# Optimization experiments

Hardware: AMD Instinct MI355X
Metric: run time of the kernel (lower is better)

Reference implementation:

```python
import jax, jax.numpy as jnp
import numpy as np

MODEL_DIM = 2048
NUM_HEADS = 32
HEAD_DIM = MODEL_DIM // NUM_HEADS
WINDOW = 512
THETA = 10000.0


def _rope_cos_sin(pos_offset, T, dim):
    # freqs_cis for positions [pos_offset, pos_offset+T); total_len <= MAX_SEQ_LEN so no rescale
    inv_freq = 1.0 / (THETA ** (jnp.arange(0, dim, 2, dtype=jnp.float32) / dim))  # [dim/2]
    t = jnp.arange(pos_offset, pos_offset + T, dtype=jnp.float32)                 # [T]
    ang = t[:, None] * inv_freq[None, :]                                          # [T, dim/2]
    return jnp.cos(ang), jnp.sin(ang)


def _apply_rope(x, cos, sin):
    # x: [B, H, T, Hd]; complex multiply on (even, odd) pairs, done in fp32 like torch code
    dt = x.dtype
    xr = x.astype(jnp.float32).reshape(*x.shape[:-1], -1, 2)
    a, b = xr[..., 0], xr[..., 1]
    c = cos[None, None, :, :]
    s = sin[None, None, :, :]
    out = jnp.stack([a * c - b * s, a * s + b * c], axis=-1).reshape(x.shape)
    return out.astype(dt)


def setup_inputs() -> dict:
    key = jax.random.key(0)
    ks = jax.random.split(key, 7)
    B, T, D = 16, 256, MODEL_DIM
    cache_len = 512
    wscale = 1.0 / np.sqrt(MODEL_DIM)
    return {
        "x": jax.random.normal(ks[0], (B, T, D), jnp.float32),
        "past_k": jax.random.normal(ks[1], (B, NUM_HEADS, cache_len, HEAD_DIM), jnp.float32),
        "past_v": jax.random.normal(ks[2], (B, NUM_HEADS, cache_len, HEAD_DIM), jnp.float32),
        "Wq": jax.random.normal(ks[3], (D, D), jnp.float32) * wscale,
        "Wk": jax.random.normal(ks[4], (D, D), jnp.float32) * wscale,
        "Wv": jax.random.normal(ks[5], (D, D), jnp.float32) * wscale,
        "Wo": jax.random.normal(ks[6], (D, D), jnp.float32) * wscale,
        "pos_offset": 512,
    }


def reference(x, past_k, past_v, Wq, Wk, Wv, Wo, pos_offset):
    B, T, D = x.shape
    H, Hd = NUM_HEADS, HEAD_DIM

    q = (x @ Wq.T).reshape(B, T, H, Hd).transpose(0, 2, 1, 3)   # [B,H,T,Hd]
    cur_k = (x @ Wk.T).reshape(B, T, H, Hd).transpose(0, 2, 1, 3)
    cur_v = (x @ Wv.T).reshape(B, T, H, Hd).transpose(0, 2, 1, 3)

    cos, sin = _rope_cos_sin(pos_offset, T, Hd)
    q = _apply_rope(q, cos, sin)
    k_rot = _apply_rope(cur_k, cos, sin)

    # KV-cache window trim (static shapes)
    cache_len = past_k.shape[2]
    sapa = max(0, cache_len - (WINDOW - T))
    k = jnp.concatenate([past_k[:, :, sapa:], k_rot], axis=2)   # [B,H,Sk,Hd]
    v = jnp.concatenate([past_v[:, :, sapa:], cur_v], axis=2)
    Sk = k.shape[2]
    past_len_visible = Sk - T

    # fp32 attention with windowed-causal mask, matching torch eager math
    scores = jnp.einsum('bhqd,bhkd->bhqk', q.astype(jnp.float32), k.astype(jnp.float32))
    scores = scores * (Hd ** -0.5)
    masked = jnp.arange(Sk)[None, :] > (jnp.arange(T)[:, None] + past_len_visible)  # [T,Sk]
    scores = jnp.where(masked[None, None], -jnp.inf, scores)
    attn = jax.nn.softmax(scores, axis=-1)
    out = jnp.einsum('bhqk,bhkd->bhqd', attn, v.astype(jnp.float32))
    out = out.transpose(0, 2, 1, 3).reshape(B, T, D) @ Wo.T
    out = out.astype(x.dtype)

    # new KV cache: full cache + UNrotated current k (faithful to source), trimmed to window
    new_k = jnp.concatenate([past_k, cur_k], axis=2)[:, :, -WINDOW:]
    new_v = jnp.concatenate([past_v, cur_v], axis=2)[:, :, -WINDOW:]
    return out, new_k, new_v
```

## Files before the change

kernel.cpp:

```cpp
#include <hip/hip_runtime.h>
#include <cstdint>
#include <cstddef>

typedef __attribute__((ext_vector_type(8))) __bf16 bf16x8;
typedef __attribute__((ext_vector_type(4))) float f32x4;

typedef const __attribute__((address_space(1))) unsigned int* gas1_t;
typedef __attribute__((address_space(3))) unsigned int* las3_t;

__device__ __forceinline__ unsigned short f2bf(float f) {
  unsigned int u = __float_as_uint(f);
  u += 0x7FFFu + ((u >> 16) & 1u);
  return (unsigned short)(u >> 16);
}
__device__ __forceinline__ float bf2f(unsigned short h) {
  return __uint_as_float(((unsigned int)h) << 16);
}

__device__ __forceinline__ int detect_f32(const unsigned short* det) {
  int cnt = 0;
#pragma unroll
  for (int i = 0; i < 32; ++i) {
    const unsigned int e = (det[2 * i] >> 7) & 0xFF;
    cnt += (e >= 115 && e <= 135) ? 1 : 0;
  }
  return cnt < 16;
}

__device__ __forceinline__ float loadf(const void* b, size_t i, int f32) {
  return f32 ? ((const float*)b)[i] : bf2f(((const unsigned short*)b)[i]);
}
__device__ __forceinline__ void storef(void* b, size_t i, float v, int f32) {
  if (f32) ((float*)b)[i] = v;
  else     ((unsigned short*)b)[i] = f2bf(v);
}
__device__ __forceinline__ bf16x8 load8(const void* base, size_t elem, int f32) {
  if (f32) {
    const float* p = (const float*)base + elem;
    const float4 a = *(const float4*)p;
    const float4 b = *(const float4*)(p + 4);
    bf16x8 r;
    unsigned short* q = (unsigned short*)&r;
    q[0] = f2bf(a.x); q[1] = f2bf(a.y); q[2] = f2bf(a.z); q[3] = f2bf(a.w);
    q[4] = f2bf(b.x); q[5] = f2bf(b.y); q[6] = f2bf(b.z); q[7] = f2bf(b.w);
    return r;
  }
  return *(const bf16x8*)((const unsigned short*)base + elem);
}

__global__ __launch_bounds__(256) void convert_kernel(
    const void* __restrict__ x,  const void* __restrict__ wq,
    const void* __restrict__ wk, const void* __restrict__ wv,
    const void* __restrict__ wo,
    unsigned short* __restrict__ xb, unsigned short* __restrict__ wqkv,
    unsigned short* __restrict__ wob, const unsigned short* __restrict__ det)
{
  const int f32 = detect_f32(det);
  int c = blockIdx.x * 256 + threadIdx.x;
#pragma unroll
  for (int it = 0; it < 3; ++it, c += 1048576) {
    bf16x8 v; unsigned short* dp;
    if (c < 1048576) {
      v = load8(x, (size_t)c << 3, f32);                     dp = xb   + ((size_t)c << 3);
    } else if (c < 1572864) {
      v = load8(wq, (size_t)(c - 1048576) << 3, f32);        dp = wqkv + ((size_t)(c - 1048576) << 3);
    } else if (c < 2097152) {
      v = load8(wk, (size_t)(c - 1572864) << 3, f32);        dp = wqkv + 4194304 + ((size_t)(c - 1572864) << 3);
    } else if (c < 2621440) {
      v = load8(wv, (size_t)(c - 2097152) << 3, f32);        dp = wqkv + 8388608 + ((size_t)(c - 2097152) << 3);
    } else {
      v = load8(wo, (size_t)(c - 2621440) << 3, f32);        dp = wob  + ((size_t)(c - 2621440) << 3);
    }
    *(bf16x8*)dp = v;
  }
}

__global__ __launch_bounds__(256) void gemm_bf16_kernel(
    const unsigned short* __restrict__ A,
    const unsigned short* __restrict__ W,
    void* __restrict__ c0,
    void* __restrict__ dko,
    const unsigned short* __restrict__ det,
    int route)
{
  __shared__ __align__(16) unsigned short As[128 * 64];
  __shared__ __align__(16) unsigned short Bs[128 * 64];
  const int f32 = detect_f32(det);

  const int tid  = threadIdx.x;
  const int lane = tid & 63;
  const int wave = tid >> 6;
  const int quad = lane >> 4;
  const int l16  = lane & 15;

  const int qq  = gridDim.x >> 3;
  const int swz = (blockIdx.x & 7) * qq + (blockIdx.x >> 3);
  const int mBase = (swz & 31) * 128;
  const int nBase = (swz >> 5) * 128;

  const int wm = (wave >> 1) * 64;
  const int wn = (wave & 1) * 64;
  const int r0w  = wave * 32;
  const int lrow = lane >> 3;
  const int lch  = (lane & 7) ^ lrow;

  f32x4 acc[4][4];
#pragma unroll
  for (int i = 0; i < 4; ++i)
#pragma unroll
    for (int j = 0; j < 4; ++j) acc[i][j] = f32x4{0.f, 0.f, 0.f, 0.f};

  const unsigned short* Abase = A + (size_t)mBase * 2048;
  const unsigned short* Wbase = W + (size_t)nBase * 2048;
  const int sa = l16 & 7;

  for (int kb = 0; kb < 2048; kb += 64) {
    __syncthreads();
#pragma unroll
    for (int ii = 0; ii < 4; ++ii) {
      const int r0 = r0w + ii * 8;
      const size_t goff = (size_t)(r0 + lrow) * 2048 + kb + lch * 8;
      __builtin_amdgcn_global_load_lds((gas1_t)(Abase + goff),
                                       (las3_t)(As + r0 * 64), 16, 0, 0);
      __builtin_amdgcn_global_load_lds((gas1_t)(Wbase + goff),
                                       (las3_t)(Bs + r0 * 64), 16, 0, 0);
    }
    __syncthreads();

    bf16x8 af[2][4], bfr[2][4];
#pragma unroll
    for (int i = 0; i < 4; ++i) {
      const char* pa = (const char*)As + (wm + i * 16 + l16) * 128;
      const char* pb = (const char*)Bs + (wn + i * 16 + l16) * 128;
      af[0][i]  = *(const bf16x8*)(pa + ((quad ^ sa) << 4));
      af[1][i]  = *(const bf16x8*)(pa + (((quad + 4) ^ sa) << 4));
      bfr[0][i] = *(const bf16x8*)(pb + ((quad ^ sa) << 4));
      bfr[1][i] = *(const bf16x8*)(pb + (((quad + 4) ^ sa) << 4));
    }
#pragma unroll
    for (int kk = 0; kk < 2; ++kk)
#pragma unroll
      for (int i = 0; i < 4; ++i)
#pragma unroll
        for (int j = 0; j < 4; ++j)
          acc[i][j] = __builtin_amdgcn_mfma_f32_16x16x32_bf16(af[kk][i], bfr[kk][j], acc[i][j], 0, 0, 0);
  }

#pragma unroll
  for (int i = 0; i < 4; ++i) {
#pragma unroll
    for (int j = 0; j < 4; ++j) {
#pragma unroll
      for (int r = 0; r < 4; ++r) {
        const int m = mBase + wm + i * 16 + quad * 4 + r;
        const int n = nBase + wn + j * 16 + l16;
        if (route == 0) {
          storef(c0, (size_t)m * 2048 + n, acc[i][j][r], f32);
        } else {
          const int b = m >> 8, t = m & 255;
          const int seg = n >> 11;
          const int nn = n & 2047;
          const int hh = nn >> 6, d = nn & 63;
          if (seg == 0) {
            ((unsigned short*)c0)[(((size_t)(b * 32 + hh)) * 256 + t) * 64 + d] =
                f2bf(acc[i][j][r]);
          } else {
            const size_t coff = (seg == 1) ? (size_t)8388608 : (size_t)25165824;
            storef(dko, coff + (((size_t)(b * 32 + hh)) * 512 + 256 + t) * 64 + d,
                   acc[i][j][r], f32);
          }
        }
      }
    }
  }
}

__global__ __launch_bounds__(256) void gemm_bt_kernel(
    const void* __restrict__ A, const void* __restrict__ W, void* __restrict__ C,
    const unsigned short* __restrict__ det,
    int amode, int wmode, int cmode, size_t coff,
    int N, int K, int mode, int S, int t0)
{
  __shared__ __align__(16) unsigned short As[128 * 32];
  __shared__ __align__(16) unsigned short Bs[128 * 32];
  const int f32  = detect_f32(det);
  const int af32 = amode & f32, wf32 = wmode & f32, cf32 = cmode & f32;

  const int tid  = threadIdx.x;
  const int lane = tid & 63;
  const int wave = tid >> 6;
  const int quad = lane >> 4;
  const int l16  = lane & 15;
  const int mBase = blockIdx.x * 128;
  const int nBase = blockIdx.y * 128;
  const int wm = (wave >> 1) * 64;
  const int wn = (wave & 1) * 64;

  const int row0 = tid >> 2,          kc0 = (tid & 3) << 3;
  const int row1 = (256 + tid) >> 2,  kc1 = ((256 + tid) & 3) << 3;

  f32x4 acc[4][4];
#pragma unroll
  for (int i = 0; i < 4; ++i)
#pragma unroll
    for (int j = 0; j < 4; ++j) acc[i][j] = f32x4{0.f, 0.f, 0.f, 0.f};

  for (int kb = 0; kb < K; kb += 32) {
    const bf16x8 a0 = load8(A, (size_t)(mBase + row0) * K + kb + kc0, af32);
    const bf16x8 a1 = load8(A, (size_t)(mBase + row1) * K + kb + kc1, af32);
    const bf16x8 b0 = load8(W, (size_t)(nBase + row0) * K + kb + kc0, wf32);
    const bf16x8 b1 = load8(W, (size_t)(nBase + row1) * K + kb + kc1, wf32);
    __syncthreads();
    *(bf16x8*)&As[(size_t)tid * 8]         = a0;
    *(bf16x8*)&As[(size_t)(256 + tid) * 8] = a1;
    *(bf16x8*)&Bs[(size_t)tid * 8]         = b0;
    *(bf16x8*)&Bs[(size_t)(256 + tid) * 8] = b1;
    __syncthreads();

    bf16x8 af[4], bfr[4];
#pragma unroll
    for (int i = 0; i < 4; ++i)
      af[i]  = *(const bf16x8*)&As[(wm + i * 16 + l16) * 32 + quad * 8];
#pragma unroll
    for (int j = 0; j < 4; ++j)
      bfr[j] = *(const bf16x8*)&Bs[(wn + j * 16 + l16) * 32 + quad * 8];
#pragma unroll
    for (int i = 0; i < 4; ++i)
#pragma unroll
      for (int j = 0; j < 4; ++j)
        acc[i][j] = __builtin_amdgcn_mfma_f32_16x16x32_bf16(af[i], bfr[j], acc[i][j], 0, 0, 0);
  }

#pragma unroll
  for (int i = 0; i < 4; ++i) {
#pragma unroll
    for (int j = 0; j < 4; ++j) {
#pragma unroll
      for (int r = 0; r < 4; ++r) {
        const int m = mBase + wm + i * 16 + quad * 4 + r;
        const int n = nBase + wn + j * 16 + l16;
        size_t idx;
        if (mode == 0) {
          idx = (size_t)m * N + n;
        } else {
          const int b = m >> 8, t = m & 255;
          const int hh = n >> 6, d = n & 63;
          idx = (((size_t)(b * 32 + hh)) * S + (t0 + t)) * 64 + d;
        }
        storef(C, coff + idx, acc[i][j][r], cf32);
      }
    }
  }
}

__global__ __launch_bounds__(256) void copy_kernel(
    const void* __restrict__ past_k, const void* __restrict__ past_v,
    void* __restrict__ dout, const unsigned short* __restrict__ det)
{
  const int f32 = detect_f32(det);
  const int es  = f32 ? 4 : 2;
  const int bh  = blockIdx.x;
  const int tid = threadIdx.x;
  const size_t srcOff  = ((size_t)bh * 512 + 256) * 64 * es;
  const size_t dstKOff = ((size_t)8388608  + (size_t)bh * 512 * 64) * es;
  const size_t dstVOff = ((size_t)25165824 + (size_t)bh * 512 * 64) * es;
  const uint4* sK = (const uint4*)((const char*)past_k + srcOff);
  const uint4* sV = (const uint4*)((const char*)past_v + srcOff);
  uint4* dK = (uint4*)((char*)dout + dstKOff);
  uint4* dV = (uint4*)((char*)dout + dstVOff);
  const int n4 = 16384 * es / 16;
  for (int c = tid; c < n4; c += 256) { dK[c] = sK[c]; dV[c] = sV[c]; }
}

__global__ __launch_bounds__(256) void rope_kernel(
    const int* __restrict__ pos_p,
    unsigned short* __restrict__ qbuf,
    const void* __restrict__ dout,
    unsigned short* __restrict__ krot,
    const unsigned short* __restrict__ det)
{
  const int f32 = detect_f32(det);
  const int gid = blockIdx.x * 256 + threadIdx.x;
  const int which = gid >> 22;
  const int pi = gid & ((1 << 22) - 1);
  const int i  = pi & 31;
  const int t  = (pi >> 5) & 255;
  const int bh = pi >> 13;
  const float pos  = (float)(*pos_p + t);
  const float freq = expf(-(float)i * 0.2878231366242557f);
  float sn, cs;
  sincosf(pos * freq, &sn, &cs);
  if (which == 0) {
    unsigned short* p = qbuf + (((size_t)bh * 256 + t) * 64 + 2 * i);
    const float a = bf2f(p[0]), b2 = bf2f(p[1]);
    p[0] = f2bf(a * cs - b2 * sn);
    p[1] = f2bf(a * sn + b2 * cs);
  } else {
    const size_t src = 8388608 + (((size_t)bh * 512 + 256 + t) * 64 + 2 * i);
    unsigned short* dp = krot + (((size_t)bh * 256 + t) * 64 + 2 * i);
    const float a = loadf(dout, src, f32), b2 = loadf(dout, src + 1, f32);
    dp[0] = f2bf(a * cs - b2 * sn);
    dp[1] = f2bf(a * sn + b2 * cs);
  }
}

__global__ __launch_bounds__(256, 1) void attn_kernel(
    const unsigned short* __restrict__ q,
    const void* __restrict__ past_k,
    const unsigned short* __restrict__ k_rot,
    const void* __restrict__ past_v,
    const void* __restrict__ dout,
    unsigned short* __restrict__ attn_out,
    const unsigned short* __restrict__ det)
{
  __shared__ __align__(16) unsigned short K_smem[512 * 64];
  __shared__ __align__(16) unsigned short Vt_smem[64 * 512];
  __shared__ __align__(16) unsigned short p_lds[4][16 * 32];

  const int f32 = detect_f32(det);
  const int bh = blockIdx.x;
  const int b  = bh >> 5;
  const int h  = bh & 31;
  const int tid  = threadIdx.x;
  const int wave = tid >> 6;
  const int lane = tid & 63;
  const int quad = lane >> 4;
  const int l16  = lane & 15;
  const float NEG = -1e30f;

  const unsigned short* qb_ptr = q + (size_t)bh * 256 * 64;
  const unsigned short* krot   = k_rot + (size_t)bh * 256 * 64;
  const size_t kpastBase = ((size_t)bh * 512 + 256) * 64;
  const size_t vpastBase = ((size_t)bh * 512 + 256) * 64;
  const size_t vcurBase  = 25165824 + (size_t)bh * 512 * 64;

#pragma unroll 4
  for (int it = 0; it < 16; ++it) {
    const int lin = it * 256 + tid;
    const int j  = lin >> 3;
    const int d0 = (lin & 7) << 3;
    bf16x8 kv, vv;
    if (j < 256) {
      kv = load8(past_k, kpastBase + (size_t)j * 64 + d0, f32);
      vv = load8(past_v, vpastBase + (size_t)j * 64 + d0, f32);
    } else {
      kv = *(const bf16x8*)&krot[(size_t)(j - 256) * 64 + d0];
      vv = load8(dout, vcurBase + (size_t)j * 64 + d0, f32);
    }
    *(bf16x8*)((char*)K_smem + (j * 128 + ((d0 * 2) ^ ((j & 7) << 4)))) = kv;
    const unsigned short* vs = (const unsigned short*)&vv;
    const int dh = (d0 >> 3) & 7;
    const int jx = j * 2;
#pragma unroll
    for (int i = 0; i < 8; ++i)
      *(unsigned short*)((char*)Vt_smem +
          ((d0 + i) * 1024 + (jx ^ ((i ^ dh) << 4)))) = vs[i];
  }
  __syncthreads();

  unsigned short* pw = p_lds[wave];
  volatile unsigned short* pwv = pw;

  for (int g = 0; g < 4; ++g) {
    const int s = (g & 1) ? (g * 4 + 3 - wave) : (g * 4 + wave);
    const int qbase = s * 16;
    const bf16x8 aq0 = *(const bf16x8*)&qb_ptr[(qbase + l16) * 64 + quad * 8];
    const bf16x8 aq1 = *(const bf16x8*)&qb_ptr[(qbase + l16) * 64 + 32 + quad * 8];
    f32x4 o[4];
#pragma unroll
    for (int nt = 0; nt < 4; ++nt) o[nt] = f32x4{0.f, 0.f, 0.f, 0.f};
    float m_i[4], l_i[4];
#pragma unroll
    for (int r = 0; r < 4; ++r) { m_i[r] = NEG; l_i[r] = 0.f; }

    const int np = ((qbase + 271) >> 5) + 1;

    for (int p = 0; p < np; ++p) {
      const int j0 = p * 32;
      f32x4 s0 = f32x4{0.f, 0.f, 0.f, 0.f};
      f32x4 s1 = f32x4{0.f, 0.f, 0.f, 0.f};
#pragma unroll
      for (int half = 0; half < 2; ++half) {
        const int j = j0 + half * 16 + l16;
        const int krow = j * 128;
        const int ksw  = (j & 7) << 4;
        const bf16x8 kb0 = *(const bf16x8*)((const char*)K_smem +
                           (krow + ((quad * 16) ^ ksw)));
        const bf16x8 kb1 = *(const bf16x8*)((const char*)K_smem +
                           (krow + ((64 + quad * 16) ^ ksw)));
        f32x4& sx = half ? s1 : s0;
        sx = __builtin_amdgcn_mfma_f32_16x16x32_bf16(aq0, kb0, sx, 0, 0, 0);
        sx = __builtin_amdgcn_mfma_f32_16x16x32_bf16(aq1, kb1, sx, 0, 0, 0);
      }
#pragma unroll
      for (int r = 0; r < 4; ++r) {
        const int qrow = qbase + quad * 4 + r;
        float v0 = s0[r] * 0.125f;
        float v1 = s1[r] * 0.125f;
        if (j0 + l16 > qrow + 256)      v0 = NEG;
        if (j0 + 16 + l16 > qrow + 256) v1 = NEG;
        float t = fmaxf(v0, v1);
        t = fmaxf(t, __shfl_xor(t, 1));
        t = fmaxf(t, __shfl_xor(t, 2));
        t = fmaxf(t, __shfl_xor(t, 4));
        t = fmaxf(t, __shfl_xor(t, 8));
        const float mnew = fmaxf(m_i[r], t);
        const float alpha = __expf(m_i[r] - mnew);
        m_i[r] = mnew;
        const float p0 = __expf(v0 - mnew);
        const float p1 = __expf(v1 - mnew);
        float rs = p0 + p1;
        rs += __shfl_xor(rs, 1);
        rs += __shfl_xor(rs, 2);
        rs += __shfl_xor(rs, 4);
        rs += __shfl_xor(rs, 8);
        l_i[r] = l_i[r] * alpha + rs;
        pwv[(quad * 4 + r) * 32 + l16]      = f2bf(p0);
        pwv[(quad * 4 + r) * 32 + 16 + l16] = f2bf(p1);
#pragma unroll
        for (int nt = 0; nt < 4; ++nt) o[nt][r] *= alpha;
      }
      asm volatile("s_waitcnt lgkmcnt(0)" ::: "memory");
      __builtin_amdgcn_sched_barrier(0);
      const bf16x8 ap = *(const bf16x8*)&pw[l16 * 32 + quad * 8];
#pragma unroll
      for (int nt = 0; nt < 4; ++nt) {
        const int d = nt * 16 + l16;
        const int vsw = ((d & 7) ^ ((d >> 3) & 7)) << 4;
        const bf16x8 bv = *(const bf16x8*)((const char*)Vt_smem +
                          (d * 1024 + (((j0 + quad * 8) * 2) ^ vsw)));
        o[nt] = __builtin_amdgcn_mfma_f32_16x16x32_bf16(ap, bv, o[nt], 0, 0, 0);
      }
    }
#pragma unroll
    for (int r = 0; r < 4; ++r) {
      const float inv = 1.0f / l_i[r];
      const int t = qbase + quad * 4 + r;
#pragma unroll
      for (int nt = 0; nt < 4; ++nt) {
        attn_out[((size_t)(b * 256 + t)) * 2048 + h * 64 + nt * 16 + l16] =
            f2bf(o[nt][r] * inv);
      }
    }
  }
}

extern "C" void kernel_launch(void* const* d_in, const int* in_sizes, int n_in,
                              void* d_out, int out_size, void* d_ws, size_t ws_size,
                              hipStream_t stream)
{
  const void* x      = d_in[0];
  const void* past_k = d_in[1];
  const void* past_v = d_in[2];
  const void* Wq     = d_in[3];
  const void* Wk     = d_in[4];
  const void* Wv     = d_in[5];
  const void* Wo     = d_in[6];
  const int* pos_p   = (const int*)d_in[7];
  const unsigned short* det = (const unsigned short*)x;

  unsigned short* ws = (unsigned short*)d_ws;
  const dim3 gb(256);

  if (ws_size >= (size_t)67108864) {
    unsigned short* q_ws    = ws;
    unsigned short* xb      = ws + 8388608;
    unsigned short* ao_ws   = ws + 8388608;
    unsigned short* wqkv    = ws + 16777216;
    unsigned short* krot_ws = ws + 16777216;
    unsigned short* wob     = ws + 29360128;

    hipLaunchKernelGGL(convert_kernel, dim3(4096), gb, 0, stream,
                       x, Wq, Wk, Wv, Wo, xb, wqkv, wob, det);
    hipLaunchKernelGGL(gemm_bf16_kernel, dim3(1536), gb, 0, stream,
                       xb, wqkv, (void*)q_ws, d_out, det, 1);
    hipLaunchKernelGGL(copy_kernel, dim3(512), gb, 0, stream, past_k, past_v, d_out, det);
    hipLaunchKernelGGL(rope_kernel, dim3(32768), gb, 0, stream, pos_p, q_ws, d_out, krot_ws, det);
    hipLaunchKernelGGL(attn_kernel, dim3(512), gb, 0, stream,
                       q_ws, past_k, krot_ws, past_v, d_out, ao_ws, det);
    hipLaunchKernelGGL(gemm_bf16_kernel, dim3(512), gb, 0, stream,
                       ao_ws, wob, d_out, d_out, det, 0);
  } else {
    unsigned short* q_ws    = ws;
    unsigned short* krot_ws = ws + 8388608;
    unsigned short* ao_ws   = ws + 16777216;
    const dim3 gg(32, 16);
    hipLaunchKernelGGL(gemm_bt_kernel, gg, gb, 0, stream, x, Wq, (void*)q_ws, det,
                       1, 1, 0, (size_t)0,        2048, 2048, 1, 256, 0);
    hipLaunchKernelGGL(gemm_bt_kernel, gg, gb, 0, stream, x, Wk, d_out, det,
                       1, 1, 1, (size_t)8388608,  2048, 2048, 1, 512, 256);
    hipLaunchKernelGGL(gemm_bt_kernel, gg, gb, 0, stream, x, Wv, d_out, det,
                       1, 1, 1, (size_t)25165824, 2048, 2048, 1, 512, 256);
    hipLaunchKernelGGL(copy_kernel, dim3(512), gb, 0, stream, past_k, past_v, d_out, det);
    hipLaunchKernelGGL(rope_kernel, dim3(32768), gb, 0, stream, pos_p, q_ws, d_out, krot_ws, det);
    hipLaunchKernelGGL(attn_kernel, dim3(512), gb, 0, stream,
                       q_ws, past_k, krot_ws, past_v, d_out, ao_ws, det);
    hipLaunchKernelGGL(gemm_bt_kernel, gg, gb, 0, stream, (const void*)ao_ws, Wo, d_out, det,
                       0, 1, 1, (size_t)0,        2048, 2048, 0, 0, 0);
  }
}
```

Measured before the change: 673.9 us.

## Double-buffer GEMM LDS tiles, fuse cache copy into convert, use fast rope intrinsics

The bf16 GEMM now moves from single-buffered 64-wide K tiles to double-buffered 32-wide K tiles, so global-to-LDS loads for the next tile overlap the MFMA work on the current one. It also uses a new swizzle, drops one barrier per step and sets a launch bound of 3 blocks per SM. The past K/V cache copy is folded into the convert kernel as extra blocks, removing one launch. The rope kernel switches to the fast __expf and __sincosf intrinsics, which trade some accuracy for speed at the large angles produced by the position offset.

Result: slower. 711.2 us (+5.5%).

```diff
diff --git a/kernel.cpp b/kernel.cpp
--- a/kernel.cpp
+++ b/kernel.cpp
@@ -52,11 +52,28 @@
     const void* __restrict__ x,  const void* __restrict__ wq,
     const void* __restrict__ wk, const void* __restrict__ wv,
     const void* __restrict__ wo,
+    const void* __restrict__ past_k, const void* __restrict__ past_v,
+    void* __restrict__ dout,
     unsigned short* __restrict__ xb, unsigned short* __restrict__ wqkv,
     unsigned short* __restrict__ wob, const unsigned short* __restrict__ det)
 {
   const int f32 = detect_f32(det);
-  int c = blockIdx.x * 256 + threadIdx.x;
+  const int tid = threadIdx.x;
+  if (blockIdx.x >= 4096) {
+    const int es  = f32 ? 4 : 2;
+    const int bh  = blockIdx.x - 4096;
+    const size_t srcOff  = ((size_t)bh * 512 + 256) * 64 * es;
+    const size_t dstKOff = ((size_t)8388608  + (size_t)bh * 512 * 64) * es;
+    const size_t dstVOff = ((size_t)25165824 + (size_t)bh * 512 * 64) * es;
+    const uint4* sK = (const uint4*)((const char*)past_k + srcOff);
+    const uint4* sV = (const uint4*)((const char*)past_v + srcOff);
+    uint4* dK = (uint4*)((char*)dout + dstKOff);
+    uint4* dV = (uint4*)((char*)dout + dstVOff);
+    const int n4 = 16384 * es / 16;
+    for (int c = tid; c < n4; c += 256) { dK[c] = sK[c]; dV[c] = sV[c]; }
+    return;
+  }
+  int c = blockIdx.x * 256 + tid;
 #pragma unroll
   for (int it = 0; it < 3; ++it, c += 1048576) {
     bf16x8 v; unsigned short* dp;
@@ -75,7 +92,7 @@
   }
 }
 
-__global__ __launch_bounds__(256) void gemm_bf16_kernel(
+__global__ __launch_bounds__(256, 3) void gemm_bf16_kernel(
     const unsigned short* __restrict__ A,
     const unsigned short* __restrict__ W,
     void* __restrict__ c0,
@@ -83,8 +100,8 @@
     const unsigned short* __restrict__ det,
     int route)
 {
-  __shared__ __align__(16) unsigned short As[128 * 64];
-  __shared__ __align__(16) unsigned short Bs[128 * 64];
+  __shared__ __align__(16) unsigned short As[2][128 * 32];
+  __shared__ __align__(16) unsigned short Bs[2][128 * 32];
   const int f32 = detect_f32(det);
 
   const int tid  = threadIdx.x;
@@ -100,9 +117,12 @@
 
   const int wm = (wave >> 1) * 64;
   const int wn = (wave & 1) * 64;
-  const int r0w  = wave * 32;
-  const int lrow = lane >> 3;
-  const int lch  = (lane & 7) ^ lrow;
+
+  const int schk = (tid & 3) ^ ((tid >> 3) & 3);
+  const unsigned short* Ap = A + (size_t)(mBase + (tid >> 2)) * 2048 + (schk << 3);
+  const unsigned short* Wp = W + (size_t)(nBase + (tid >> 2)) * 2048 + (schk << 3);
+
+  const int rdOff = ((quad ^ ((l16 >> 1) & 3)) << 4);
 
   f32x4 acc[4][4];
 #pragma unroll
@@ -110,41 +130,48 @@
 #pragma unroll
     for (int j = 0; j < 4; ++j) acc[i][j] = f32x4{0.f, 0.f, 0.f, 0.f};
 
-  const unsigned short* Abase = A + (size_t)mBase * 2048;
-  const unsigned short* Wbase = W + (size_t)nBase * 2048;
-  const int sa = l16 & 7;
-
-  for (int kb = 0; kb < 2048; kb += 64) {
+#define STAGE(bufi, kb) do {                                                   \
+    __builtin_amdgcn_global_load_lds((gas1_t)(Ap + (kb)),                      \
+        (las3_t)&As[bufi][tid * 8], 16, 0, 0);                                 \
+    __builtin_amdgcn_global_load_lds((gas1_t)(Ap + (kb) + 131072),             \
+        (las3_t)&As[bufi][2048 + tid * 8], 16, 0, 0);                          \
+    __builtin_amdgcn_global_load_lds((gas1_t)(Wp + (kb)),                      \
+        (las3_t)&Bs[bufi][tid * 8], 16, 0, 0);                                 \
+    __builtin_amdgcn_global_load_lds((gas1_t)(Wp + (kb) + 131072),             \
+        (las3_t)&Bs[bufi][2048 + tid * 8], 16, 0, 0);                          \
+  } while (0)
+
+#define COMPUTE(bufi) do {                                                     \
+    bf16x8 af[4], bfr[4];                                                      \
+    const char* baseA = (const char*)&As[bufi][0];                             \
+    const char* baseB = (const char*)&Bs[bufi][0];                             \
+    _Pragma("unroll")                                                          \
+    for (int i = 0; i < 4; ++i) {                                              \
+      af[i]  = *(const bf16x8*)(baseA + (wm + i * 16 + l16) * 64 + rdOff);     \
+      bfr[i] = *(const bf16x8*)(baseB + (wn + i * 16 + l16) * 64 + rdOff);     \
+    }                                                                          \
+    _Pragma("unroll")                                                          \
+    for (int i = 0; i < 4; ++i)                                                \
+      _Pragma("unroll")                                                        \
+      for (int j = 0; j < 4; ++j)                                              \
+        acc[i][j] = __builtin_amdgcn_mfma_f32_16x16x32_bf16(af[i], bfr[j],     \
+                                                            acc[i][j], 0, 0, 0); \
+  } while (0)
+
+  STAGE(0, 0);
+  __syncthreads();
+  int cur = 0;
+#pragma unroll 2
+  for (int t = 1; t < 64; ++t) {
+    STAGE(cur ^ 1, t * 32);
+    COMPUTE(cur);
     __syncthreads();
-#pragma unroll
-    for (int ii = 0; ii < 4; ++ii) {
-      const int r0 = r0w + ii * 8;
-      const size_t goff = (size_t)(r0 + lrow) * 2048 + kb + lch * 8;
-      __builtin_amdgcn_global_load_lds((gas1_t)(Abase + goff),
-                                       (las3_t)(As + r0 * 64), 16, 0, 0);
-      __builtin_amdgcn_global_load_lds((gas1_t)(Wbase + goff),
-                                       (las3_t)(Bs + r0 * 64), 16, 0, 0);
-    }
-    __syncthreads();
-
-    bf16x8 af[2][4], bfr[2][4];
-#pragma unroll
-    for (int i = 0; i < 4; ++i) {
-      const char* pa = (const char*)As + (wm + i * 16 + l16) * 128;
-      const char* pb = (const char*)Bs + (wn + i * 16 + l16) * 128;
-      af[0][i]  = *(const bf16x8*)(pa + ((quad ^ sa) << 4));
-      af[1][i]  = *(const bf16x8*)(pa + (((quad + 4) ^ sa) << 4));
-      bfr[0][i] = *(const bf16x8*)(pb + ((quad ^ sa) << 4));
-      bfr[1][i] = *(const bf16x8*)(pb + (((quad + 4) ^ sa) << 4));
-    }
-#pragma unroll
-    for (int kk = 0; kk < 2; ++kk)
-#pragma unroll
-      for (int i = 0; i < 4; ++i)
-#pragma unroll
-        for (int j = 0; j < 4; ++j)
-          acc[i][j] = __builtin_amdgcn_mfma_f32_16x16x32_bf16(af[kk][i], bfr[kk][j], acc[i][j], 0, 0, 0);
-  }
+    cur ^= 1;
+  }
+  COMPUTE(cur);
+
+#undef STAGE
+#undef COMPUTE
 
 #pragma unroll
   for (int i = 0; i < 4; ++i) {
@@ -287,9 +314,9 @@
   const int t  = (pi >> 5) & 255;
   const int bh = pi >> 13;
   const float pos  = (float)(*pos_p + t);
-  const float freq = expf(-(float)i * 0.2878231366242557f);
+  const float freq = __expf(-(float)i * 0.2878231366242557f);
   float sn, cs;
-  sincosf(pos * freq, &sn, &cs);
+  __sincosf(pos * freq, &sn, &cs);
   if (which == 0) {
     unsigned short* p = qbuf + (((size_t)bh * 256 + t) * 64 + 2 * i);
     const float a = bf2f(p[0]), b2 = bf2f(p[1]);
@@ -470,11 +497,11 @@
     unsigned short* krot_ws = ws + 16777216;
     unsigned short* wob     = ws + 29360128;
 
-    hipLaunchKernelGGL(convert_kernel, dim3(4096), gb, 0, stream,
-                       x, Wq, Wk, Wv, Wo, xb, wqkv, wob, det);
+    hipLaunchKernelGGL(convert_kernel, dim3(4608), gb, 0, stream,
+                       x, Wq, Wk, Wv, Wo, past_k, past_v, d_out,
+                       xb, wqkv, wob, det);
     hipLaunchKernelGGL(gemm_bf16_kernel, dim3(1536), gb, 0, stream,
                        xb, wqkv, (void*)q_ws, d_out, det, 1);
-    hipLaunchKernelGGL(copy_kernel, dim3(512), gb, 0, stream, past_k, past_v, d_out, det);
     hipLaunchKernelGGL(rope_kernel, dim3(32768), gb, 0, stream, pos_p, q_ws, d_out, krot_ws, det);
     hipLaunchKernelGGL(attn_kernel, dim3(512), gb, 0, stream,
                        q_ws, past_k, krot_ws, past_v, d_out, ao_ws, det);
```
